# Optimization experiments

Measured on AMD Instinct MI355X. Metric: run time of the kernel, lower is better.

The kernel has to match this reference:

```python
import jax, jax.numpy as jnp
from jax import lax
import numpy as np

B, CIN, HC, K, REC = 64, 64, 64, 3, 5
MG = 240 // REC  # 48
EPS = 1e-8


def conv2d(x, w, b, pad):
    y = lax.conv_general_dilated(x, w, (1, 1), [(pad, pad), (pad, pad)],
                                 dimension_numbers=('NCHW', 'OIHW', 'NCHW'))
    return y + b[None, :, None, None]


def conv_transpose2d(x, w, b, stride, pad):
    # PyTorch ConvTranspose2d: w is (Cin, Cout, kH, kW)
    k = w.shape[2]
    w_t = jnp.transpose(w[:, :, ::-1, ::-1], (1, 0, 2, 3))  # -> OIHW, flipped
    y = lax.conv_general_dilated(x, w_t, (1, 1),
                                 [(k - 1 - pad, k - 1 - pad)] * 2,
                                 lhs_dilation=(stride, stride),
                                 dimension_numbers=('NCHW', 'OIHW', 'NCHW'))
    return y + b[None, :, None, None]


def leaky(x):
    return jnp.where(x >= 0, x, 0.2 * x)


def setup_inputs() -> dict:
    key = jax.random.key(0)
    ks = jax.random.split(key, 12)
    s = 0.05
    return {
        'x': jax.random.normal(ks[0], (B, CIN, 64, 64), jnp.float32),
        'h': jax.random.normal(ks[1], (B, HC, 64, 64), jnp.float32),
        'c': jax.random.normal(ks[2], (B, HC, 64, 64), jnp.float32),
        'recalled_memory_feature': jax.random.normal(ks[3], (B, REC, MG, 32, 32), jnp.float32),
        'conv_w': jax.random.normal(ks[4], (5 * HC, CIN + HC, K, K), jnp.float32) * s,
        'conv_b': jax.random.normal(ks[5], (5 * HC,), jnp.float32) * s,
        'convc_w': jax.random.normal(ks[6], (MG, HC, 1, 1), jnp.float32) * s,
        'convc_b': jax.random.normal(ks[7], (MG,), jnp.float32) * s,
        'convssm_w': jax.random.normal(ks[8], (MG, MG, 4, 4), jnp.float32) * s,
        'convssm_b': jax.random.normal(ks[9], (MG,), jnp.float32) * s,
        'convfuse_w': jax.random.normal(ks[10], (HC, MG + HC, 1, 1), jnp.float32) * s,
        'convfuse_b': jax.random.normal(ks[11], (HC,), jnp.float32) * s,
    }


def reference(x, h, c, recalled_memory_feature, conv_w, conv_b, convc_w, convc_b,
              convssm_w, convssm_b, convfuse_w, convfuse_b):
    rm = recalled_memory_feature.reshape(B, REC, MG, 32, 32)
    rm_avg = rm.mean(axis=(3, 4))                      # (B, REC, MG)
    q = leaky(conv2d(c, convc_w, convc_b, 0))          # (B, MG, 64, 64)
    q_avg = q.mean(axis=(2, 3))                        # (B, MG)
    # cosine similarity along channel dim, vectorized over (B, REC)
    qn = jnp.maximum(jnp.linalg.norm(q_avg, axis=1, keepdims=True), EPS)   # (B,1)
    mn = jnp.maximum(jnp.linalg.norm(rm_avg, axis=2), EPS)                  # (B,REC)
    cos = jnp.einsum('bm,brm->br', q_avg, rm_avg) / (qn * mn)               # (B,REC)
    attn = jax.nn.softmax(cos, axis=1)                                      # (B,REC)
    mt = jnp.einsum('br,brmhw->bmhw', attn, rm)        # (B, MG, 32, 32)
    mt = leaky(conv_transpose2d(mt, convssm_w, convssm_b, 2, 1))  # (B, MG, 64, 64)

    gates = conv2d(jnp.concatenate((x, h), axis=1), conv_w, conv_b, K // 2)
    i, f, g, o, lam = jnp.split(gates, 5, axis=1)
    i = jax.nn.sigmoid(i)
    f = jax.nn.sigmoid(f)
    o = jax.nn.sigmoid(o)
    g = jnp.tanh(g)
    lam = jax.nn.sigmoid(lam)
    c_new = f * c + i * g
    h_new = o * jnp.tanh(conv2d(jnp.concatenate((c_new, mt), axis=1), convfuse_w, convfuse_b, 0))
    h_out = lam * h_new + (1.0 - lam) * h
    return (h_out, c_new)
```

## Files before the change

### kernel.cpp

```cpp
#include <hip/hip_runtime.h>
#include <hip/hip_bf16.h>
#include <cstdint>

#define HW 4096
#define MGc 48
#define RECc 5

typedef __attribute__((ext_vector_type(8))) short bf16x8;
typedef __attribute__((ext_vector_type(4))) float f32x4;

__device__ __forceinline__ float sigf(float x) { return 1.f / (1.f + expf(-x)); }
__device__ __forceinline__ float leakyf(float x) { return x >= 0.f ? x : 0.2f * x; }
__device__ __forceinline__ unsigned short f2bfu(float f) {
  __hip_bfloat16 b = __float2bfloat16(f);
  return *reinterpret_cast<unsigned short*>(&b);
}
__device__ __forceinline__ float bfu2f(unsigned short u) {
  unsigned v = ((unsigned)u) << 16;
  return __uint_as_float(v);
}
__device__ __forceinline__ void gload_lds16(const void* g, void* l) {
  __builtin_amdgcn_global_load_lds(
      (const __attribute__((address_space(1))) unsigned int*)g,
      (__attribute__((address_space(3))) unsigned int*)l, 16, 0, 0);
}
__device__ __forceinline__ void fma4(f32x4& a, float w, const f32x4& v) {
  a[0] += w * v[0]; a[1] += w * v[1]; a[2] += w * v[2]; a[3] += w * v[3];
}

__global__ __launch_bounds__(256) void k_att(const float* __restrict__ rm,
    float* __restrict__ rm_sum, const float* __restrict__ c,
    const float* __restrict__ ccw, const float* __restrict__ ccb,
    float* __restrict__ q_part) {
  __shared__ __align__(16) char smem[13568];
  int bid = blockIdx.x, tid = threadIdx.x;
  if (bid < 15360) {
    float* sred = (float*)smem;
    int row = bid;
    const float4* p = reinterpret_cast<const float4*>(rm + (size_t)row * 1024);
    float4 v = p[tid];
    float s = v.x + v.y + v.z + v.w;
    #pragma unroll
    for (int off = 32; off; off >>= 1) s += __shfl_down(s, off);
    if ((tid & 63) == 0) sred[tid >> 6] = s;
    __syncthreads();
    if (tid == 0) rm_sum[row] = sred[0] + sred[1] + sred[2] + sred[3];
  } else {
    float* wl = (float*)smem;
    float* bl = wl + MGc * 64;
    float (*red)[MGc] = (float(*)[MGc])(bl + 64);
    int r = bid - 15360;
    int seg = r & 15, b = r >> 4;
    for (int i = tid; i < MGc * 64; i += 256) wl[i] = ccw[i];
    if (tid < MGc) bl[tid] = ccb[tid];
    __syncthreads();
    int px = seg * 256 + tid;
    float acc[MGc];
    #pragma unroll
    for (int m = 0; m < MGc; m++) acc[m] = 0.f;
    const float* cp = c + (size_t)b * 64 * HW + px;
    for (int ci = 0; ci < 64; ci++) {
      float v = cp[(size_t)ci * HW];
      #pragma unroll
      for (int m = 0; m < MGc; m++) acc[m] += wl[m * 64 + ci] * v;
    }
    int lane = tid & 63, wv = tid >> 6;
    #pragma unroll
    for (int m = 0; m < MGc; m++) {
      float t2 = leakyf(acc[m] + bl[m]);
      #pragma unroll
      for (int off = 32; off; off >>= 1) t2 += __shfl_down(t2, off);
      if (lane == 0) red[wv][m] = t2;
    }
    __syncthreads();
    if (tid < MGc) {
      float t2 = red[0][tid] + red[1][tid] + red[2][tid] + red[3][tid];
      q_part[((size_t)b * 16 + seg) * MGc + tid] = t2;
    }
  }
}

__global__ __launch_bounds__(256) void k_mid(const float* __restrict__ rm,
    const float* __restrict__ rm_sum, const float* __restrict__ q_part,
    float* __restrict__ mt_pre, const float* __restrict__ cw,
    __hip_bfloat16* __restrict__ Wp, __hip_bfloat16* __restrict__ Pp,
    const float* __restrict__ xin, const float* __restrict__ hin) {
  __shared__ __align__(16) char smem[16704];
  int bid = blockIdx.x, tid = threadIdx.x;
  if (bid < 12288) {
    float* sat = (float*)smem;
    int idx = bid * 256 + tid;
    int b = idx / (MGc * 1024);
    if (tid < 64) {
      int lane = tid;
      float q = 0.f;
      if (lane < MGc) {
        float s = 0.f;
        for (int sg = 0; sg < 16; sg++) s += q_part[((size_t)b * 16 + sg) * MGc + lane];
        q = s * (1.f / 4096.f);
      }
      float qs = q * q;
      #pragma unroll
      for (int off = 32; off; off >>= 1) qs += __shfl_xor(qs, off);
      float qn = fmaxf(sqrtf(qs), 1e-8f);
      float cosv[RECc];
      #pragma unroll
      for (int r = 0; r < RECc; r++) {
        float m = 0.f;
        if (lane < MGc) m = rm_sum[((size_t)b * RECc + r) * MGc + lane] * (1.f / 1024.f);
        float d = q * m, ms = m * m;
        #pragma unroll
        for (int off = 32; off; off >>= 1) { d += __shfl_xor(d, off); ms += __shfl_xor(ms, off); }
        float mn = fmaxf(sqrtf(ms), 1e-8f);
        cosv[r] = d / (qn * mn);
      }
      float mx = cosv[0];
      #pragma unroll
      for (int r = 1; r < RECc; r++) mx = fmaxf(mx, cosv[r]);
      float ssum = 0.f;
      #pragma unroll
      for (int r = 0; r < RECc; r++) { cosv[r] = expf(cosv[r] - mx); ssum += cosv[r]; }
      float inv = 1.f / ssum;
      #pragma unroll
      for (int r = 0; r < RECc; r++)
        if (lane == r) sat[r] = cosv[r] * inv;
    }
    __syncthreads();
    int rem = idx - b * (MGc * 1024);
    const float* base = rm + (size_t)b * RECc * MGc * 1024 + rem;
    float v = sat[0] * base[0] + sat[1] * base[MGc * 1024] + sat[2] * base[2 * MGc * 1024]
            + sat[3] * base[3 * MGc * 1024] + sat[4] * base[4 * MGc * 1024];
    mt_pre[idx] = v;
  } else if (bid < 13728) {
    int idx = (bid - 12288) * 256 + tid;
    int t = idx / (320 * 128);
    int rem = idx % (320 * 128);
    int ocp = rem / 128, ci = rem % 128;
    int nt = ocp / 80, r2 = ocp % 80, gate = r2 / 16, ml = r2 % 16;
    int oc = gate * 64 + nt * 16 + ml;
    Wp[idx] = __float2bfloat16(cw[((size_t)oc * 128 + ci) * 9 + t]);
  } else if (bid < 14768) {
    int idx = (bid - 13728) * 256 + tid;
    int b = idx / 4160, i = idx % 4160;
    bf16x8* base = reinterpret_cast<bf16x8*>(Pp);
    size_t u;
    if (i < 2112) {
      int r = (i < 1056) ? 0 : 65;
      int j = (i < 1056) ? i : i - 1056;
      u = ((size_t)b * 66 + r) * 1056 + j;
    } else {
      int i2 = i - 2112;
      int row = 1 + (i2 >> 5), k = i2 & 31;
      int px = (k < 16) ? 0 : 65, ci8 = k & 15;
      u = (((size_t)b * 66 + row) * 66 + px) * 16 + ci8;
    }
    base[u] = (bf16x8)0;
  } else {
    float (*t)[65] = (float(*)[65])smem;
    int r = bid - 14768;
    int half = r & 1, y = (r >> 1) & 63, b = r >> 7;
    const float* src = (half ? hin : xin) + (size_t)b * 64 * HW + y * 64;
    #pragma unroll
    for (int it = 0; it < 4; it++) {
      int li = it * 256 + tid;
      int ci = li >> 4, x4 = (li & 15) * 4;
      float4 v = *reinterpret_cast<const float4*>(src + (size_t)ci * HW + x4);
      t[x4][ci] = v.x; t[x4 + 1][ci] = v.y; t[x4 + 2][ci] = v.z; t[x4 + 3][ci] = v.w;
    }
    __syncthreads();
    int x = tid >> 2, c16 = (tid & 3) * 16;
    unsigned short* dst = reinterpret_cast<unsigned short*>(Pp) +
        ((((size_t)b * 66 + y + 1) * 66 + x + 1) * 128 + half * 64 + c16);
    bf16x8 o0, o1;
    #pragma unroll
    for (int j = 0; j < 8; j++) {
      o0[j] = (short)f2bfu(t[x][c16 + j]);
      o1[j] = (short)f2bfu(t[x][c16 + 8 + j]);
    }
    *reinterpret_cast<bf16x8*>(dst) = o0;
    *reinterpret_cast<bf16x8*>(dst + 8) = o1;
  }
}

__global__ __launch_bounds__(256) void k_main(
    const __hip_bfloat16* __restrict__ Pp, const __hip_bfloat16* __restrict__ Wp,
    const float* __restrict__ c, const float* __restrict__ cb,
    float* __restrict__ c_new, __hip_bfloat16* __restrict__ o_g,
    __hip_bfloat16* __restrict__ lam_g,
    const float* __restrict__ mt_pre, const float* __restrict__ sw,
    const float* __restrict__ sb, __hip_bfloat16* __restrict__ mt) {
  __shared__ __align__(16) char arena[66816];
  int bid = blockIdx.x, tid = threadIdx.x;
  if (bid < 4096) {
    bf16x8* s_in = (bf16x8*)arena;
    bf16x8* s_w  = (bf16x8*)(arena + 20736);
    int t_id = (bid & 7) * 512 + (bid >> 3);
    int b = t_id >> 6;
    int r6 = t_id & 63;
    int ytile = r6 >> 4, xtile = (r6 >> 2) & 3, nt = r6 & 3;
    int y0 = ytile * 16, x0 = xtile * 16;
    int wv = tid >> 6, lane = tid & 63;
    int lane15 = lane & 15, lq = lane >> 4;

    const char* Pb = (const char*)Pp;
    const char* Wb = (const char*)Wp;

    const char* gin[6]; int din[6]; bool ain[6];
    #pragma unroll
    for (int k = 0; k < 6; k++) {
      int u = wv + 4 * k;
      int e = u * 64 + lane;
      ain[k] = (u < 21) && (e < 1296);
      int ee = (e < 1296) ? e : 0;
      int L = ee / 72, r = ee - L * 72;
      int llq = r / 18, xi = r - llq * 18;
      gin[k] = Pb + ((((size_t)b * 66 + y0 + L) * 66 + (x0 + xi)) * 256) + llq * 16;
      din[k] = ee;
    }
    const char* gw[12]; int dw[12]; bool aw[12];
    #pragma unroll
    for (int k = 0; k < 12; k++) {
      int u = wv + 4 * k;
      aw[k] = (u < 45);
      int uu = (u < 45) ? u : 0;
      int e = uu * 64 + lane;
      int unit = e / 80, ol = e - unit * 80;
      int t = unit >> 2, g = unit & 3;
      gw[k] = Wb + (((size_t)t * 320 + nt * 80 + ol) * 128 + g * 8) * 2;
      dw[k] = e;
    }

    f32x4 acc[4][5];
    #pragma unroll
    for (int i = 0; i < 4; i++)
      #pragma unroll
      for (int j = 0; j < 5; j++) acc[i][j] = (f32x4)0.f;

    #pragma unroll 1
    for (int cc = 0; cc < 4; cc++) {
      __syncthreads();
      int co = cc * 64;
      #pragma unroll
      for (int k = 0; k < 6; k++)
        if (ain[k]) gload_lds16(gin[k] + co, (void*)&s_in[din[k]]);
      #pragma unroll
      for (int k = 0; k < 12; k++)
        if (aw[k]) gload_lds16(gw[k] + co, (void*)&s_w[dw[k]]);
      __syncthreads();

      #pragma unroll
      for (int dx = 0; dx < 3; dx++) {
        bf16x8 af[6];
        #pragma unroll
        for (int r = 0; r < 6; r++)
          af[r] = s_in[((wv * 4 + r) * 4 + lq) * 18 + lane15 + dx];
        #pragma unroll
        for (int ky = 0; ky < 3; ky++) {
          int t = ky * 3 + dx;
          bf16x8 bw[5];
          #pragma unroll
          for (int gg = 0; gg < 5; gg++)
            bw[gg] = s_w[(t * 4 + lq) * 80 + gg * 16 + lane15];
          __builtin_amdgcn_s_setprio(1);
          #pragma unroll
          for (int rr = 0; rr < 4; rr++)
            #pragma unroll
            for (int gg = 0; gg < 5; gg++)
              acc[rr][gg] = __builtin_amdgcn_mfma_f32_16x16x32_bf16(
                  af[rr + ky], bw[gg], acc[rr][gg], 0, 0, 0);
          __builtin_amdgcn_s_setprio(0);
        }
      }
    }

    int m_hid = nt * 16 + lane15;
    float bi = cb[m_hid], bff = cb[64 + m_hid], bgg = cb[128 + m_hid],
          bo = cb[192 + m_hid], bl = cb[256 + m_hid];
    int xb = x0 + lq * 4;
    size_t chofs = ((size_t)b * 64 + m_hid) * HW;
    #pragma unroll
    for (int rr = 0; rr < 4; rr++) {
      int y = y0 + wv * 4 + rr;
      size_t pofs = chofs + (size_t)y * 64 + xb;
      f32x4 cold = *reinterpret_cast<const f32x4*>(c + pofs);
      f32x4 cn;
      unsigned short ov[4], lv[4];
      #pragma unroll
      for (int e = 0; e < 4; e++) {
        float i_ = sigf(acc[rr][0][e] + bi);
        float f_ = sigf(acc[rr][1][e] + bff);
        float g_ = tanhf(acc[rr][2][e] + bgg);
        float o_ = sigf(acc[rr][3][e] + bo);
        float l_ = sigf(acc[rr][4][e] + bl);
        cn[e] = f_ * cold[e] + i_ * g_;
        ov[e] = f2bfu(o_);
        lv[e] = f2bfu(l_);
      }
      *reinterpret_cast<f32x4*>(c_new + pofs) = cn;
      ushort4 ovv = {ov[0], ov[1], ov[2], ov[3]};
      ushort4 lvv = {lv[0], lv[1], lv[2], lv[3]};
      *reinterpret_cast<ushort4*>(reinterpret_cast<unsigned short*>(o_g) + pofs) = ovv;
      *reinterpret_cast<ushort4*>(reinterpret_cast<unsigned short*>(lam_g) + pofs) = lvv;
    }
  } else {
    float (*in_t)[10][20] = (float(*)[10][20])arena;
    float (*w_t)[48][16]  = (float(*)[48][16])(arena + 9600);
    int sbid = bid - 4096;
    int tile = sbid & 7, b = sbid >> 3;
    int y0 = (tile >> 1) * 16, x0 = (tile & 1) * 32;
    int wv = tid >> 6, lane = tid & 63;
    int co0 = wv * 12;
    int oyl = lane >> 2, xseg = lane & 3;
    int oy = y0 + oyl;
    int iy0 = (y0 >> 1) - 1, ix0 = (x0 >> 1) - 1;
    int kyA = (oy + 1) & 1;
    int iyA = (oy + 1 - kyA) >> 1;
    int rA = iyA - iy0, rB = rA - 1;
    float acc[12][8] = {};
    for (int ch = 0; ch < 4; ch++) {
      int ci0 = ch * 12;
      __syncthreads();
      for (int i = tid; i < 12 * 10 * 18; i += 256) {
        int ci = i / 180, rr = (i % 180) / 18, cc2 = i % 18;
        int giy = iy0 + rr, gix = ix0 + cc2;
        float v = 0.f;
        if ((unsigned)giy < 32u && (unsigned)gix < 32u)
          v = mt_pre[(((size_t)b * MGc + ci0 + ci) * 32 + giy) * 32 + gix];
        in_t[ci][rr][cc2] = v;
      }
      for (int i = tid; i < 12 * 48 * 16; i += 256)
        (&w_t[0][0][0])[i] = sw[ci0 * 768 + i];
      __syncthreads();
      #pragma unroll 1
      for (int ci = 0; ci < 12; ci++) {
        float4 a0 = *reinterpret_cast<const float4*>(&in_t[ci][rA][xseg * 4]);
        float4 a1 = *reinterpret_cast<const float4*>(&in_t[ci][rA][xseg * 4 + 4]);
        float4 b0 = *reinterpret_cast<const float4*>(&in_t[ci][rB][xseg * 4]);
        float4 b1 = *reinterpret_cast<const float4*>(&in_t[ci][rB][xseg * 4 + 4]);
        float vA[6] = {a0.x, a0.y, a0.z, a0.w, a1.x, a1.y};
        float vB[6] = {b0.x, b0.y, b0.z, b0.w, b1.x, b1.y};
        #pragma unroll
        for (int co = 0; co < 12; co++) {
          const float* wp = &w_t[ci][co0 + co][0];
          float4 wA = *reinterpret_cast<const float4*>(wp + kyA * 4);
          float4 wB = *reinterpret_cast<const float4*>(wp + (kyA + 2) * 4);
          #pragma unroll
          for (int j = 0; j < 8; j++) {
            if ((j & 1) == 0) {
              int hi = (j >> 1) + 1, lo = j >> 1;
              acc[co][j] += vA[hi] * wA.y + vA[lo] * wA.w + vB[hi] * wB.y + vB[lo] * wB.w;
            } else {
              int hi = ((j + 1) >> 1) + 1, lo = (j + 1) >> 1;
              acc[co][j] += vA[hi] * wA.x + vA[lo] * wA.z + vB[hi] * wB.x + vB[lo] * wB.z;
            }
          }
        }
      }
    }
    int oxb = x0 + xseg * 8;
    #pragma unroll
    for (int co = 0; co < 12; co++) {
      float bb = sb[co0 + co];
      size_t obase = (((size_t)b * MGc + co0 + co) * 64 + oy) * 64 + oxb;
      #pragma unroll
      for (int j = 0; j < 8; j++)
        mt[obase + j] = __float2bfloat16(leakyf(acc[co][j] + bb));
    }
  }
}

__global__ __launch_bounds__(256) void k_fuse(const float* __restrict__ c_new,
    const __hip_bfloat16* __restrict__ mt, const __hip_bfloat16* __restrict__ o_g,
    const __hip_bfloat16* __restrict__ lam_g, const float* __restrict__ h,
    const float* __restrict__ fw, const float* __restrict__ fb,
    float* __restrict__ h_out) {
  __shared__ float wl[112][32];
  int b = blockIdx.y;
  int seg = blockIdx.x & 3, chalf = blockIdx.x >> 2;
  int co0 = chalf * 32;
  for (int i = threadIdx.x; i < 112 * 32; i += 256) {
    int ci = i >> 5, co = i & 31;
    wl[ci][co] = fw[(co0 + co) * 112 + ci];
  }
  __syncthreads();
  int px = seg * 1024 + threadIdx.x * 4;
  size_t bofs = (size_t)b * 64 * HW;
  f32x4 acc[32];
  #pragma unroll
  for (int co = 0; co < 32; co++) acc[co] = (f32x4)(fb[co0 + co]);
  #pragma unroll 1
  for (int ci = 0; ci < 64; ci++) {
    f32x4 v = *reinterpret_cast<const f32x4*>(c_new + bofs + (size_t)ci * HW + px);
    #pragma unroll
    for (int c4 = 0; c4 < 8; c4++) {
      float4 w = *reinterpret_cast<const float4*>(&wl[ci][c4 * 4]);
      fma4(acc[c4 * 4 + 0], w.x, v);
      fma4(acc[c4 * 4 + 1], w.y, v);
      fma4(acc[c4 * 4 + 2], w.z, v);
      fma4(acc[c4 * 4 + 3], w.w, v);
    }
  }
  const unsigned short* mtu = reinterpret_cast<const unsigned short*>(mt);
  size_t mtofs = (size_t)b * MGc * HW + px;
  #pragma unroll 1
  for (int ci = 0; ci < 48; ci++) {
    ushort4 u = *reinterpret_cast<const ushort4*>(mtu + mtofs + (size_t)ci * HW);
    f32x4 v;
    v[0] = bfu2f(u.x); v[1] = bfu2f(u.y); v[2] = bfu2f(u.z); v[3] = bfu2f(u.w);
    #pragma unroll
    for (int c4 = 0; c4 < 8; c4++) {
      float4 w = *reinterpret_cast<const float4*>(&wl[64 + ci][c4 * 4]);
      fma4(acc[c4 * 4 + 0], w.x, v);
      fma4(acc[c4 * 4 + 1], w.y, v);
      fma4(acc[c4 * 4 + 2], w.z, v);
      fma4(acc[c4 * 4 + 3], w.w, v);
    }
  }
  const unsigned short* ou = reinterpret_cast<const unsigned short*>(o_g);
  const unsigned short* lu = reinterpret_cast<const unsigned short*>(lam_g);
  #pragma unroll
  for (int co = 0; co < 32; co++) {
    size_t ofs = bofs + (size_t)(co0 + co) * HW + px;
    ushort4 uo = *reinterpret_cast<const ushort4*>(ou + ofs);
    ushort4 ul = *reinterpret_cast<const ushort4*>(lu + ofs);
    f32x4 hv = *reinterpret_cast<const f32x4*>(h + ofs);
    const unsigned short* uop = &uo.x;
    const unsigned short* ulp = &ul.x;
    f32x4 r;
    #pragma unroll
    for (int e = 0; e < 4; e++) {
      float hn = tanhf(acc[co][e]);
      float o = bfu2f(uop[e]);
      float l = bfu2f(ulp[e]);
      r[e] = l * (o * hn) + (1.f - l) * hv[e];
    }
    *reinterpret_cast<f32x4*>(h_out + ofs) = r;
  }
}

extern "C" void kernel_launch(void* const* d_in, const int* in_sizes, int n_in,
                              void* d_out, int out_size, void* d_ws, size_t ws_size,
                              hipStream_t stream) {
  const float* x   = (const float*)d_in[0];
  const float* h   = (const float*)d_in[1];
  const float* c   = (const float*)d_in[2];
  const float* rm  = (const float*)d_in[3];
  const float* cw  = (const float*)d_in[4];
  const float* cb  = (const float*)d_in[5];
  const float* ccw = (const float*)d_in[6];
  const float* ccb = (const float*)d_in[7];
  const float* sw  = (const float*)d_in[8];
  const float* sb  = (const float*)d_in[9];
  const float* fw  = (const float*)d_in[10];
  const float* fb  = (const float*)d_in[11];

  float* h_out = (float*)d_out;
  float* c_new = h_out + (size_t)16777216;

  char* ws = (char*)d_ws;
  float* rm_sum = (float*)(ws + 0);
  float* q_part = (float*)(ws + 65536);
  __hip_bfloat16* o_g   = (__hip_bfloat16*)(ws + 0);
  __hip_bfloat16* lam_g = (__hip_bfloat16*)(ws + 33554432);
  __hip_bfloat16* mt    = (__hip_bfloat16*)(ws + 67108864);
  __hip_bfloat16* Pp    = (__hip_bfloat16*)(ws + 92274688);
  __hip_bfloat16* Wp    = (__hip_bfloat16*)(ws + 163643392);
  float* mt_pre = h_out;

  k_att<<<16384, 256, 0, stream>>>(rm, rm_sum, c, ccw, ccb, q_part);
  k_mid<<<22960, 256, 0, stream>>>(rm, rm_sum, q_part, mt_pre, cw, Wp, Pp, x, h);
  k_main<<<4608, 256, 0, stream>>>(Pp, Wp, c, cb, c_new, o_g, lam_g, mt_pre, sw, sb, mt);
  k_fuse<<<dim3(8, 64), 256, 0, stream>>>(c_new, mt, o_g, lam_g, h, fw, fb, h_out);
}
```

Measured before the change: 635.7 us.

## Split fused gates/SSM kernel into separate launches with wider SSM blocks

Splits the combined k_main kernel, which branched on block index between the MFMA gate convolution and the transposed-conv SSM path, into two kernels launched one after the other. The SSM kernel now uses 512-thread blocks with 6 output channels per wave instead of 12, which lowers register pressure and the per-thread serial work. The gate kernel keeps its tiling but gets a statically sized LDS allocation rather than the shared arena. The cost is an extra launch and losing the overlap of the 512 SSM blocks with the tail of the gate blocks.

Result: no change. 639.8 us (+0.7%).

```diff
diff --git a/kernel.cpp b/kernel.cpp
--- a/kernel.cpp
+++ b/kernel.cpp
@@ -182,190 +182,190 @@
   }
 }
 
-__global__ __launch_bounds__(256) void k_main(
+__global__ __launch_bounds__(512) void k_ssm(const float* __restrict__ mt_pre,
+    const float* __restrict__ w, const float* __restrict__ bias,
+    __hip_bfloat16* __restrict__ mt) {
+  __shared__ float in_t[12][10][20];
+  __shared__ float w_t[12][48][16];
+  int b = blockIdx.y;
+  int tile = blockIdx.x;
+  int y0 = (tile >> 1) * 16, x0 = (tile & 1) * 32;
+  int wv = threadIdx.x >> 6, lane = threadIdx.x & 63;
+  int co0 = wv * 6;
+  int oyl = lane >> 2, xseg = lane & 3;
+  int oy = y0 + oyl;
+  int iy0 = (y0 >> 1) - 1, ix0 = (x0 >> 1) - 1;
+  int kyA = (oy + 1) & 1;
+  int iyA = (oy + 1 - kyA) >> 1;
+  int rA = iyA - iy0, rB = rA - 1;
+  float acc[6][8] = {};
+  for (int ch = 0; ch < 4; ch++) {
+    int ci0 = ch * 12;
+    __syncthreads();
+    for (int i = threadIdx.x; i < 12 * 10 * 18; i += 512) {
+      int ci = i / 180, rr = (i % 180) / 18, cc2 = i % 18;
+      int giy = iy0 + rr, gix = ix0 + cc2;
+      float v = 0.f;
+      if ((unsigned)giy < 32u && (unsigned)gix < 32u)
+        v = mt_pre[(((size_t)b * MGc + ci0 + ci) * 32 + giy) * 32 + gix];
+      in_t[ci][rr][cc2] = v;
+    }
+    for (int i = threadIdx.x; i < 12 * 48 * 16; i += 512)
+      (&w_t[0][0][0])[i] = w[ci0 * 768 + i];
+    __syncthreads();
+    #pragma unroll 1
+    for (int ci = 0; ci < 12; ci++) {
+      float4 a0 = *reinterpret_cast<const float4*>(&in_t[ci][rA][xseg * 4]);
+      float4 a1 = *reinterpret_cast<const float4*>(&in_t[ci][rA][xseg * 4 + 4]);
+      float4 b0 = *reinterpret_cast<const float4*>(&in_t[ci][rB][xseg * 4]);
+      float4 b1 = *reinterpret_cast<const float4*>(&in_t[ci][rB][xseg * 4 + 4]);
+      float vA[6] = {a0.x, a0.y, a0.z, a0.w, a1.x, a1.y};
+      float vB[6] = {b0.x, b0.y, b0.z, b0.w, b1.x, b1.y};
+      #pragma unroll
+      for (int co = 0; co < 6; co++) {
+        const float* wp = &w_t[ci][co0 + co][0];
+        float4 wA = *reinterpret_cast<const float4*>(wp + kyA * 4);
+        float4 wB = *reinterpret_cast<const float4*>(wp + (kyA + 2) * 4);
+        #pragma unroll
+        for (int j = 0; j < 8; j++) {
+          if ((j & 1) == 0) {
+            int hi = (j >> 1) + 1, lo = j >> 1;
+            acc[co][j] += vA[hi] * wA.y + vA[lo] * wA.w + vB[hi] * wB.y + vB[lo] * wB.w;
+          } else {
+            int hi = ((j + 1) >> 1) + 1, lo = (j + 1) >> 1;
+            acc[co][j] += vA[hi] * wA.x + vA[lo] * wA.z + vB[hi] * wB.x + vB[lo] * wB.z;
+          }
+        }
+      }
+    }
+  }
+  int oxb = x0 + xseg * 8;
+  #pragma unroll
+  for (int co = 0; co < 6; co++) {
+    float bb = bias[co0 + co];
+    size_t obase = (((size_t)b * MGc + co0 + co) * 64 + oy) * 64 + oxb;
+    #pragma unroll
+    for (int j = 0; j < 8; j++)
+      mt[obase + j] = __float2bfloat16(leakyf(acc[co][j] + bb));
+  }
+}
+
+__global__ __launch_bounds__(256) void k_gates_mfma(
     const __hip_bfloat16* __restrict__ Pp, const __hip_bfloat16* __restrict__ Wp,
     const float* __restrict__ c, const float* __restrict__ cb,
     float* __restrict__ c_new, __hip_bfloat16* __restrict__ o_g,
-    __hip_bfloat16* __restrict__ lam_g,
-    const float* __restrict__ mt_pre, const float* __restrict__ sw,
-    const float* __restrict__ sb, __hip_bfloat16* __restrict__ mt) {
-  __shared__ __align__(16) char arena[66816];
-  int bid = blockIdx.x, tid = threadIdx.x;
-  if (bid < 4096) {
-    bf16x8* s_in = (bf16x8*)arena;
-    bf16x8* s_w  = (bf16x8*)(arena + 20736);
-    int t_id = (bid & 7) * 512 + (bid >> 3);
-    int b = t_id >> 6;
-    int r6 = t_id & 63;
-    int ytile = r6 >> 4, xtile = (r6 >> 2) & 3, nt = r6 & 3;
-    int y0 = ytile * 16, x0 = xtile * 16;
-    int wv = tid >> 6, lane = tid & 63;
-    int lane15 = lane & 15, lq = lane >> 4;
-
-    const char* Pb = (const char*)Pp;
-    const char* Wb = (const char*)Wp;
-
-    const char* gin[6]; int din[6]; bool ain[6];
-    #pragma unroll
-    for (int k = 0; k < 6; k++) {
-      int u = wv + 4 * k;
-      int e = u * 64 + lane;
-      ain[k] = (u < 21) && (e < 1296);
-      int ee = (e < 1296) ? e : 0;
-      int L = ee / 72, r = ee - L * 72;
-      int llq = r / 18, xi = r - llq * 18;
-      gin[k] = Pb + ((((size_t)b * 66 + y0 + L) * 66 + (x0 + xi)) * 256) + llq * 16;
-      din[k] = ee;
-    }
-    const char* gw[12]; int dw[12]; bool aw[12];
-    #pragma unroll
-    for (int k = 0; k < 12; k++) {
-      int u = wv + 4 * k;
-      aw[k] = (u < 45);
-      int uu = (u < 45) ? u : 0;
-      int e = uu * 64 + lane;
-      int unit = e / 80, ol = e - unit * 80;
-      int t = unit >> 2, g = unit & 3;
-      gw[k] = Wb + (((size_t)t * 320 + nt * 80 + ol) * 128 + g * 8) * 2;
-      dw[k] = e;
-    }
-
-    f32x4 acc[4][5];
-    #pragma unroll
-    for (int i = 0; i < 4; i++)
-      #pragma unroll
-      for (int j = 0; j < 5; j++) acc[i][j] = (f32x4)0.f;
-
-    #pragma unroll 1
-    for (int cc = 0; cc < 4; cc++) {
-      __syncthreads();
-      int co = cc * 64;
-      #pragma unroll
-      for (int k = 0; k < 6; k++)
-        if (ain[k]) gload_lds16(gin[k] + co, (void*)&s_in[din[k]]);
-      #pragma unroll
-      for (int k = 0; k < 12; k++)
-        if (aw[k]) gload_lds16(gw[k] + co, (void*)&s_w[dw[k]]);
-      __syncthreads();
-
-      #pragma unroll
-      for (int dx = 0; dx < 3; dx++) {
-        bf16x8 af[6];
+    __hip_bfloat16* __restrict__ lam_g) {
+  __shared__ bf16x8 s_in[1296];
+  __shared__ bf16x8 s_w[2880];
+  int orig = blockIdx.y * gridDim.x + blockIdx.x;
+  int t_id = (orig & 7) * 512 + (orig >> 3);
+  int b = t_id >> 6;
+  int r6 = t_id & 63;
+  int ytile = r6 >> 4, xtile = (r6 >> 2) & 3, nt = r6 & 3;
+  int y0 = ytile * 16, x0 = xtile * 16;
+  int tid = threadIdx.x;
+  int wv = tid >> 6, lane = tid & 63;
+  int lane15 = lane & 15, lq = lane >> 4;
+
+  const char* Pb = (const char*)Pp;
+  const char* Wb = (const char*)Wp;
+
+  const char* gin[6]; int din[6]; bool ain[6];
+  #pragma unroll
+  for (int k = 0; k < 6; k++) {
+    int u = wv + 4 * k;
+    int e = u * 64 + lane;
+    ain[k] = (u < 21) && (e < 1296);
+    int ee = (e < 1296) ? e : 0;
+    int L = ee / 72, r = ee - L * 72;
+    int llq = r / 18, xi = r - llq * 18;
+    gin[k] = Pb + ((((size_t)b * 66 + y0 + L) * 66 + (x0 + xi)) * 256) + llq * 16;
+    din[k] = ee;
+  }
+  const char* gw[12]; int dw[12]; bool aw[12];
+  #pragma unroll
+  for (int k = 0; k < 12; k++) {
+    int u = wv + 4 * k;
+    aw[k] = (u < 45);
+    int uu = (u < 45) ? u : 0;
+    int e = uu * 64 + lane;
+    int unit = e / 80, ol = e - unit * 80;
+    int t = unit >> 2, g = unit & 3;
+    gw[k] = Wb + (((size_t)t * 320 + nt * 80 + ol) * 128 + g * 8) * 2;
+    dw[k] = e;
+  }
+
+  f32x4 acc[4][5];
+  #pragma unroll
+  for (int i = 0; i < 4; i++)
+    #pragma unroll
+    for (int j = 0; j < 5; j++) acc[i][j] = (f32x4)0.f;
+
+  #pragma unroll 1
+  for (int cc = 0; cc < 4; cc++) {
+    __syncthreads();
+    int co = cc * 64;
+    #pragma unroll
+    for (int k = 0; k < 6; k++)
+      if (ain[k]) gload_lds16(gin[k] + co, (void*)&s_in[din[k]]);
+    #pragma unroll
+    for (int k = 0; k < 12; k++)
+      if (aw[k]) gload_lds16(gw[k] + co, (void*)&s_w[dw[k]]);
+    __syncthreads();
+
+    #pragma unroll
+    for (int dx = 0; dx < 3; dx++) {
+      bf16x8 af[6];
+      #pragma unroll
+      for (int r = 0; r < 6; r++)
+        af[r] = s_in[((wv * 4 + r) * 4 + lq) * 18 + lane15 + dx];
+      #pragma unroll
+      for (int ky = 0; ky < 3; ky++) {
+        int t = ky * 3 + dx;
+        bf16x8 bw[5];
         #pragma unroll
-        for (int r = 0; r < 6; r++)
-          af[r] = s_in[((wv * 4 + r) * 4 + lq) * 18 + lane15 + dx];
+        for (int gg = 0; gg < 5; gg++)
+          bw[gg] = s_w[(t * 4 + lq) * 80 + gg * 16 + lane15];
+        __builtin_amdgcn_s_setprio(1);
         #pragma unroll
-        for (int ky = 0; ky < 3; ky++) {
-          int t = ky * 3 + dx;
-          bf16x8 bw[5];
+        for (int rr = 0; rr < 4; rr++)
           #pragma unroll
           for (int gg = 0; gg < 5; gg++)
-            bw[gg] = s_w[(t * 4 + lq) * 80 + gg * 16 + lane15];
-          __builtin_amdgcn_s_setprio(1);
-          #pragma unroll
-          for (int rr = 0; rr < 4; rr++)
-            #pragma unroll
-            for (int gg = 0; gg < 5; gg++)
-              acc[rr][gg] = __builtin_amdgcn_mfma_f32_16x16x32_bf16(
-                  af[rr + ky], bw[gg], acc[rr][gg], 0, 0, 0);
-          __builtin_amdgcn_s_setprio(0);
-        }
+            acc[rr][gg] = __builtin_amdgcn_mfma_f32_16x16x32_bf16(
+                af[rr + ky], bw[gg], acc[rr][gg], 0, 0, 0);
+        __builtin_amdgcn_s_setprio(0);
       }
     }
-
-    int m_hid = nt * 16 + lane15;
-    float bi = cb[m_hid], bff = cb[64 + m_hid], bgg = cb[128 + m_hid],
-          bo = cb[192 + m_hid], bl = cb[256 + m_hid];
-    int xb = x0 + lq * 4;
-    size_t chofs = ((size_t)b * 64 + m_hid) * HW;
-    #pragma unroll
-    for (int rr = 0; rr < 4; rr++) {
-      int y = y0 + wv * 4 + rr;
-      size_t pofs = chofs + (size_t)y * 64 + xb;
-      f32x4 cold = *reinterpret_cast<const f32x4*>(c + pofs);
-      f32x4 cn;
-      unsigned short ov[4], lv[4];
-      #pragma unroll
-      for (int e = 0; e < 4; e++) {
-        float i_ = sigf(acc[rr][0][e] + bi);
-        float f_ = sigf(acc[rr][1][e] + bff);
-        float g_ = tanhf(acc[rr][2][e] + bgg);
-        float o_ = sigf(acc[rr][3][e] + bo);
-        float l_ = sigf(acc[rr][4][e] + bl);
-        cn[e] = f_ * cold[e] + i_ * g_;
-        ov[e] = f2bfu(o_);
-        lv[e] = f2bfu(l_);
-      }
-      *reinterpret_cast<f32x4*>(c_new + pofs) = cn;
-      ushort4 ovv = {ov[0], ov[1], ov[2], ov[3]};
-      ushort4 lvv = {lv[0], lv[1], lv[2], lv[3]};
-      *reinterpret_cast<ushort4*>(reinterpret_cast<unsigned short*>(o_g) + pofs) = ovv;
-      *reinterpret_cast<ushort4*>(reinterpret_cast<unsigned short*>(lam_g) + pofs) = lvv;
-    }
-  } else {
-    float (*in_t)[10][20] = (float(*)[10][20])arena;
-    float (*w_t)[48][16]  = (float(*)[48][16])(arena + 9600);
-    int sbid = bid - 4096;
-    int tile = sbid & 7, b = sbid >> 3;
-    int y0 = (tile >> 1) * 16, x0 = (tile & 1) * 32;
-    int wv = tid >> 6, lane = tid & 63;
-    int co0 = wv * 12;
-    int oyl = lane >> 2, xseg = lane & 3;
-    int oy = y0 + oyl;
-    int iy0 = (y0 >> 1) - 1, ix0 = (x0 >> 1) - 1;
-    int kyA = (oy + 1) & 1;
-    int iyA = (oy + 1 - kyA) >> 1;
-    int rA = iyA - iy0, rB = rA - 1;
-    float acc[12][8] = {};
-    for (int ch = 0; ch < 4; ch++) {
-      int ci0 = ch * 12;
-      __syncthreads();
-      for (int i = tid; i < 12 * 10 * 18; i += 256) {
-        int ci = i / 180, rr = (i % 180) / 18, cc2 = i % 18;
-        int giy = iy0 + rr, gix = ix0 + cc2;
-        float v = 0.f;
-        if ((unsigned)giy < 32u && (unsigned)gix < 32u)
-          v = mt_pre[(((size_t)b * MGc + ci0 + ci) * 32 + giy) * 32 + gix];
-        in_t[ci][rr][cc2] = v;
-      }
-      for (int i = tid; i < 12 * 48 * 16; i += 256)
-        (&w_t[0][0][0])[i] = sw[ci0 * 768 + i];
-      __syncthreads();
-      #pragma unroll 1
-      for (int ci = 0; ci < 12; ci++) {
-        float4 a0 = *reinterpret_cast<const float4*>(&in_t[ci][rA][xseg * 4]);
-        float4 a1 = *reinterpret_cast<const float4*>(&in_t[ci][rA][xseg * 4 + 4]);
-        float4 b0 = *reinterpret_cast<const float4*>(&in_t[ci][rB][xseg * 4]);
-        float4 b1 = *reinterpret_cast<const float4*>(&in_t[ci][rB][xseg * 4 + 4]);
-        float vA[6] = {a0.x, a0.y, a0.z, a0.w, a1.x, a1.y};
-        float vB[6] = {b0.x, b0.y, b0.z, b0.w, b1.x, b1.y};
-        #pragma unroll
-        for (int co = 0; co < 12; co++) {
-          const float* wp = &w_t[ci][co0 + co][0];
-          float4 wA = *reinterpret_cast<const float4*>(wp + kyA * 4);
-          float4 wB = *reinterpret_cast<const float4*>(wp + (kyA + 2) * 4);
-          #pragma unroll
-          for (int j = 0; j < 8; j++) {
-            if ((j & 1) == 0) {
-              int hi = (j >> 1) + 1, lo = j >> 1;
-              acc[co][j] += vA[hi] * wA.y + vA[lo] * wA.w + vB[hi] * wB.y + vB[lo] * wB.w;
-            } else {
-              int hi = ((j + 1) >> 1) + 1, lo = (j + 1) >> 1;
-              acc[co][j] += vA[hi] * wA.x + vA[lo] * wA.z + vB[hi] * wB.x + vB[lo] * wB.z;
-            }
-          }
-        }
-      }
-    }
-    int oxb = x0 + xseg * 8;
-    #pragma unroll
-    for (int co = 0; co < 12; co++) {
-      float bb = sb[co0 + co];
-      size_t obase = (((size_t)b * MGc + co0 + co) * 64 + oy) * 64 + oxb;
-      #pragma unroll
-      for (int j = 0; j < 8; j++)
-        mt[obase + j] = __float2bfloat16(leakyf(acc[co][j] + bb));
-    }
+  }
+
+  int m_hid = nt * 16 + lane15;
+  float bi = cb[m_hid], bff = cb[64 + m_hid], bgg = cb[128 + m_hid],
+        bo = cb[192 + m_hid], bl = cb[256 + m_hid];
+  int xb = x0 + lq * 4;
+  size_t chofs = ((size_t)b * 64 + m_hid) * HW;
+  #pragma unroll
+  for (int rr = 0; rr < 4; rr++) {
+    int y = y0 + wv * 4 + rr;
+    size_t pofs = chofs + (size_t)y * 64 + xb;
+    f32x4 cold = *reinterpret_cast<const f32x4*>(c + pofs);
+    f32x4 cn;
+    unsigned short ov[4], lv[4];
+    #pragma unroll
+    for (int e = 0; e < 4; e++) {
+      float i_ = sigf(acc[rr][0][e] + bi);
+      float f_ = sigf(acc[rr][1][e] + bff);
+      float g_ = tanhf(acc[rr][2][e] + bgg);
+      float o_ = sigf(acc[rr][3][e] + bo);
+      float l_ = sigf(acc[rr][4][e] + bl);
+      cn[e] = f_ * cold[e] + i_ * g_;
+      ov[e] = f2bfu(o_);
+      lv[e] = f2bfu(l_);
+    }
+    *reinterpret_cast<f32x4*>(c_new + pofs) = cn;
+    ushort4 ovv = {ov[0], ov[1], ov[2], ov[3]};
+    ushort4 lvv = {lv[0], lv[1], lv[2], lv[3]};
+    *reinterpret_cast<ushort4*>(reinterpret_cast<unsigned short*>(o_g) + pofs) = ovv;
+    *reinterpret_cast<ushort4*>(reinterpret_cast<unsigned short*>(lam_g) + pofs) = lvv;
   }
 }
 
@@ -469,6 +469,7 @@
 
   k_att<<<16384, 256, 0, stream>>>(rm, rm_sum, c, ccw, ccb, q_part);
   k_mid<<<22960, 256, 0, stream>>>(rm, rm_sum, q_part, mt_pre, cw, Wp, Pp, x, h);
-  k_main<<<4608, 256, 0, stream>>>(Pp, Wp, c, cb, c_new, o_g, lam_g, mt_pre, sw, sb, mt);
+  k_ssm<<<dim3(8, 64), 512, 0, stream>>>(mt_pre, sw, sb, mt);
+  k_gates_mfma<<<dim3(64, 64), 256, 0, stream>>>(Pp, Wp, c, cb, c_new, o_g, lam_g);
   k_fuse<<<dim3(8, 64), 256, 0, stream>>>(c_new, mt, o_g, lam_g, h, fw, fb, h_out);
 }
```
